# Optimization experiments

Hardware: AMD Instinct MI355X
Metric: run time of the kernel (lower is better)

## Reference

```python
import jax, jax.numpy as jnp
import numpy as np

N_BLADES = 32  # Cl(4,1) has 2^5 = 32 basis blades


def _gp_sign_bitwise(a, b):
    """Sign of e_a * e_b in Cl(4,1) via bitwise swap counting (numpy, static)."""
    a = np.asarray(a, dtype=np.int64)
    b = np.asarray(b, dtype=np.int64)
    a, b = np.broadcast_arrays(a, b)
    swaps = np.zeros(a.shape, dtype=np.int64)
    for i in range(5):
        b_has_i = (b >> i) & 1
        mask_gt = (~((1 << (i + 1)) - 1)) & 31
        val = a & mask_gt
        pc = (val & 1) + ((val >> 1) & 1) + ((val >> 2) & 1) + ((val >> 3) & 1) + ((val >> 4) & 1)
        swaps += b_has_i * pc
    comm_sign = np.where(swaps % 2 == 0, 1.0, -1.0)
    metric_sign = np.where(((a & 16) & (b & 16)) > 0, -1.0, 1.0)
    return (comm_sign * metric_sign).astype(np.float32)


_M = np.arange(N_BLADES)
PERM = (_M[:, None] ^ _M[None, :]).astype(np.int32)        # PERM[k, m] = m ^ k
SIGNS = _gp_sign_bitwise(_M[None, :], PERM)                 # sign(m, m^k), [32, 32]
PERM_J = jnp.asarray(PERM)
SIGNS_J = jnp.asarray(SIGNS)


def setup_inputs() -> dict:
    key = jax.random.key(0)
    kx, kw = jax.random.split(key)
    B, In, Out = 1024, 256, 256
    x = jax.random.normal(kx, (B, In, N_BLADES), dtype=jnp.float32)
    std = 0.5 / (In * N_BLADES) ** 0.5
    weight = jax.random.normal(kw, (Out, In, N_BLADES), dtype=jnp.float32) * std
    return {"x": x, "weight": weight}


def reference(x, weight):
    # x: [B, In, 32], weight: [Out, In, 32]
    # out[b, o, k] = sum_{i, m} x[b, i, m^k] * sign(m, m^k) * w[o, i, m]
    x_g = x[..., PERM_J] * SIGNS_J                 # [B, In, 32(k), 32(m)]
    out = jnp.einsum('bikm,oim->bok', x_g, weight)  # [B, Out, 32]
    return out
```

## Files before the change

kernel.cpp:

```cpp
#include <hip/hip_runtime.h>

typedef __attribute__((ext_vector_type(8))) short bf16x8;
typedef __attribute__((ext_vector_type(4))) float f32x4;
typedef __attribute__((ext_vector_type(8))) unsigned short ushort8;

#define N_BLADES 32
#define B_DIM 1024
#define IN_DIM 256
#define OUT_DIM 256
#define K_DIM (IN_DIM * N_BLADES)
#define N_DIM (OUT_DIM * N_BLADES)


__device__ __forceinline__ unsigned short f2bf(float f) {
    unsigned int u = __float_as_uint(f);
    u = (u + 0x7fff + ((u >> 16) & 1)) >> 16;
    return (unsigned short)u;
}

__device__ __forceinline__ float gp_sign(int a, int b) {
    int swaps = 0;
#pragma unroll
    for (int i = 0; i < 5; ++i) {
        int mask = (~((1 << (i + 1)) - 1)) & 31;
        swaps += ((b >> i) & 1) * __popc(a & mask);
    }
    float s = (swaps & 1) ? -1.0f : 1.0f;
    if (a & b & 16) s = -s;
    return s;
}

__device__ __forceinline__ void gload_lds16(const void* g, void* l) {
    __builtin_amdgcn_global_load_lds(
        (const __attribute__((address_space(1))) unsigned int*)g,
        (__attribute__((address_space(3))) unsigned int*)l, 16, 0, 0);
}

#define FENCE() asm volatile("" ::: "memory")
#define BAR()    { FENCE(); __builtin_amdgcn_s_barrier(); FENCE(); }
#define SCHED0() __builtin_amdgcn_sched_barrier(0)
#define LGKM(n)  { asm volatile("s_waitcnt lgkmcnt(" #n ")" ::: "memory"); SCHED0(); }
#define VMC(n)   { asm volatile("s_waitcnt vmcnt(" #n ")" ::: "memory"); SCHED0(); }
#define PRIO1()  __builtin_amdgcn_s_setprio(1)
#define PRIO0()  __builtin_amdgcn_s_setprio(0)

__global__ __launch_bounds__(256) void cast_kernel(const float4* __restrict__ x,
                                                   unsigned short* __restrict__ xb) {
    int t = blockIdx.x * 256 + threadIdx.x;
    float4 a = x[t * 2];
    float4 b = x[t * 2 + 1];
    ushort8 pk;
    pk[0] = f2bf(a.x); pk[1] = f2bf(a.y); pk[2] = f2bf(a.z); pk[3] = f2bf(a.w);
    pk[4] = f2bf(b.x); pk[5] = f2bf(b.y); pk[6] = f2bf(b.z); pk[7] = f2bf(b.w);
    *(ushort8*)(xb + (size_t)t * 8) = pk;
}

__device__ __forceinline__ bf16x8 shuffle_sign(bf16x8 v, int jx,
                                               unsigned int m0, unsigned int m1,
                                               unsigned int m2, unsigned int m3) {
    union { bf16x8 v8; unsigned int w[4]; } a, b;
    a.v8 = v;
    int s = jx >> 1;
    unsigned int t0 = (s & 1) ? a.w[1] : a.w[0];
    unsigned int t1 = (s & 1) ? a.w[0] : a.w[1];
    unsigned int t2 = (s & 1) ? a.w[3] : a.w[2];
    unsigned int t3 = (s & 1) ? a.w[2] : a.w[3];
    unsigned int u0 = (s & 2) ? t2 : t0;
    unsigned int u1 = (s & 2) ? t3 : t1;
    unsigned int u2 = (s & 2) ? t0 : t2;
    unsigned int u3 = (s & 2) ? t1 : t3;
    if (jx & 1) {
        u0 = (u0 >> 16) | (u0 << 16);
        u1 = (u1 >> 16) | (u1 << 16);
        u2 = (u2 >> 16) | (u2 << 16);
        u3 = (u3 >> 16) | (u3 << 16);
    }
    b.w[0] = u0 ^ m0; b.w[1] = u1 ^ m1; b.w[2] = u2 ^ m2; b.w[3] = u3 ^ m3;
    return b.v8;
}


#define ABUF 16384
#define TBUF 49152
#define ROWB 16384

__global__ __launch_bounds__(512, 1) void gemm_ko_kernel(const unsigned short* __restrict__ xb,
                                                         const unsigned short* __restrict__ wb,
                                                         float* __restrict__ Cws) {
    __shared__ char lds[3 * TBUF];

    const int tid  = threadIdx.x;
    const int lane = tid & 63;
    const int wid  = tid >> 6;
    const int wr   = wid >> 2;
    const int wc   = wid & 3;
    const int l15  = lane & 15;
    const int l4   = lane >> 4;
    const int swzf = (l15 & 7) << 4;

    const int  kblk = blockIdx.x;
    const long row0 = (long)blockIdx.y * 128;
    const int  jx   = kblk & 7;
    const int  khi  = kblk & 24;

    const int rowA = tid >> 2;
    const int h0   = (2 * tid) & 7;
    const int q0   = h0 & 3, q1 = (h0 + 1) & 3;
    const int aoff0 = ((h0 >> 2) * 64) + (((q0 * 8) ^ khi) * 2);
    const int aoff1 = (((h0 + 1) >> 2) * 64) + (((q1 * 8) ^ khi) * 2);
    const int adst0 = rowA * 128 + ((h0 * 16) ^ ((rowA & 7) << 4));
    const int adst1 = rowA * 128 + (((h0 + 1) * 16) ^ ((rowA & 7) << 4));
    const char* aSrcK = (const char*)xb + (row0 + rowA) * ROWB;

    unsigned int mA00, mA01, mA02, mA03, mA10, mA11, mA12, mA13;
    {
        unsigned int mk[2][4];
#pragma unroll
        for (int u = 0; u < 2; ++u) {
            int q = u ? q1 : q0;
#pragma unroll
            for (int w = 0; w < 4; ++w) {
                unsigned int mword = 0;
#pragma unroll
                for (int e2 = 0; e2 < 2; ++e2) {
                    int m = 8 * q + 2 * w + e2;
                    if (gp_sign(m, m ^ kblk) < 0.0f) mword |= 0x8000u << (16 * e2);
                }
                mk[u][w] = mword;
            }
        }
        mA00 = mk[0][0]; mA01 = mk[0][1]; mA02 = mk[0][2]; mA03 = mk[0][3];
        mA10 = mk[1][0]; mA11 = mk[1][1]; mA12 = mk[1][2]; mA13 = mk[1][3];
    }

    const int  rrB   = tid >> 3;
    const int  tid16 = tid * 16;
    const int  scbB  = ((tid & 7) * 16) ^ ((rrB & 7) << 4);
    const char* bSrc = (const char*)wb + (long)rrB * ROWB + scbB;

    char* buf0 = lds;
    char* buf1 = lds + TBUF;
    char* buf2 = lds + 2 * TBUF;

#define B_STAGE(nbuf, kpb) { \
    _Pragma("unroll") for (int n = 0; n < 4; ++n) \
        gload_lds16(bSrc + (long)n * (64L * ROWB) + (kpb), (char*)(nbuf) + ABUF + n * 8192 + tid16); }
#define A_LOAD(kpb) { \
    rA0 = *(const bf16x8*)(aSrcK + (kpb) + aoff0); \
    rA1 = *(const bf16x8*)(aSrcK + (kpb) + aoff1); }
#define A_SHUF_WRITE(nbuf) { \
    bf16x8 s0 = shuffle_sign(rA0, jx, mA00, mA01, mA02, mA03); \
    bf16x8 s1 = shuffle_sign(rA1, jx, mA10, mA11, mA12, mA13); \
    *(bf16x8*)((char*)(nbuf) + adst0) = s0; \
    *(bf16x8*)((char*)(nbuf) + adst1) = s1; }
#define READ_AB(pbuf, kk, AS, BS) { \
    _Pragma("unroll") for (int mi = 0; mi < 4; ++mi) { \
        int r = wr * 64 + mi * 16 + l15; \
        AS[mi] = *(const bf16x8*)((const char*)(pbuf) + r * 128 + (((kk) * 64 + l4 * 16) ^ swzf)); } \
    _Pragma("unroll") for (int ni = 0; ni < 4; ++ni) { \
        int r = wc * 64 + ni * 16 + l15; \
        BS[ni] = *(const bf16x8*)((const char*)(pbuf) + ABUF + r * 128 + (((kk) * 64 + l4 * 16) ^ swzf)); } }
#define MFMA16(AS, BS) \
    _Pragma("unroll") for (int mi = 0; mi < 4; ++mi) \
    _Pragma("unroll") for (int ni = 0; ni < 4; ++ni) \
        acc[mi][ni] = __builtin_amdgcn_mfma_f32_16x16x32_bf16(AS[mi], BS[ni], acc[mi][ni], 0, 0, 0);

    f32x4 acc[4][4];
#pragma unroll
    for (int mi = 0; mi < 4; ++mi)
#pragma unroll
        for (int ni = 0; ni < 4; ++ni) acc[mi][ni] = (f32x4)0.0f;

    bf16x8 rA0, rA1;
    bf16x8 aF0[4], bF0[4], aF1[4], bF1[4];

    A_LOAD(0);
    VMC(0);
    A_SHUF_WRITE(buf0);
    SCHED0();
    B_STAGE(buf0, 0);
    SCHED0();
    A_LOAD(128);
    SCHED0();
    B_STAGE(buf1, 128);
    SCHED0();
    VMC(6);
    LGKM(0);
    BAR();

    char* pc = buf0; char* pn = buf1; char* ps = buf2;
    int kp = 256;
    for (int t = 0; t < 128; ++t) {
        READ_AB(pc, 0, aF0, bF0);
        SCHED0();
        READ_AB(pc, 1, aF1, bF1);
        VMC(4);
        A_SHUF_WRITE(pn);
        SCHED0();
        A_LOAD(kp);
        SCHED0();
        B_STAGE(ps, kp);
        SCHED0();
        LGKM(10); PRIO1(); MFMA16(aF0, bF0); PRIO0();
        LGKM(2);  PRIO1(); MFMA16(aF1, bF1); PRIO0();
        VMC(6);
        LGKM(0);
        BAR();

        char* tmp = pc; pc = pn; pn = ps; ps = tmp;
        kp += 128;
        if (kp == 16384) kp = 0;
    }

    const int cr = l4 * 4;
#pragma unroll
    for (int mi = 0; mi < 4; ++mi)
#pragma unroll
        for (int ni = 0; ni < 4; ++ni)
#pragma unroll
            for (int jj = 0; jj < 4; ++jj) {
                long r = row0 + wr * 64 + mi * 16 + cr + jj;
                int  c = kblk * 256 + wc * 64 + ni * 16 + l15;
                Cws[r * N_DIM + c] = acc[mi][ni][jj];
            }

#undef B_STAGE
#undef A_LOAD
#undef A_SHUF_WRITE
#undef READ_AB
#undef MFMA16
}

__global__ __launch_bounds__(256) void transpose_kernel(const float* __restrict__ Cws,
                                                        float* __restrict__ out) {
    __shared__ float t[32 * 260];
    const int tid = threadIdx.x;
    const long b  = blockIdx.x;
    const float4* src = (const float4*)(Cws + b * N_DIM);
    float4*       dst = (float4*)(out + b * N_DIM);
#pragma unroll
    for (int r = 0; r < 8; ++r) {
        int f = tid + r * 256;
        float4 v = src[f];
        int k  = f >> 6;
        int c4 = (f & 63) * 4;
        *(float4*)&t[k * 260 + c4] = v;
    }
    __syncthreads();
#pragma unroll
    for (int r = 0; r < 8; ++r) {
        int g  = tid + r * 256;
        int o  = g >> 3;
        int k0 = (g & 7) * 4;
        float4 v;
        v.x = t[(k0 + 0) * 260 + o];
        v.y = t[(k0 + 1) * 260 + o];
        v.z = t[(k0 + 2) * 260 + o];
        v.w = t[(k0 + 3) * 260 + o];
        dst[g] = v;
    }
}

__global__ __launch_bounds__(256) void fallback_gp_kernel(const float* __restrict__ x,
                                                          const float* __restrict__ w,
                                                          float* __restrict__ out) {
    __shared__ float xs[IN_DIM * 32];
    __shared__ float tab[1024];
    int tid = threadIdx.x;
    for (int idx = tid; idx < 1024; idx += 256) {
        int m = idx >> 5, k = idx & 31;
        tab[idx] = gp_sign(m, m ^ k);
    }
    int b = blockIdx.x;
    const float4* xrow = (const float4*)(x + (long)b * K_DIM);
    float4* xs4 = (float4*)xs;
    for (int idx = tid; idx < 2048; idx += 256) xs4[idx] = xrow[idx];
    __syncthreads();

    int wid = tid >> 6, lane = tid & 63;
    int o = blockIdx.y * 8 + wid;
    int k = lane & 31, half = lane >> 5;
    float acc = 0.f;
    const float* wrow = w + (long)o * K_DIM + half * 4096;
    for (int i = 0; i < 128; ++i) {
        int ib = (half * 128 + i) * 32;
#pragma unroll
        for (int m = 0; m < 32; ++m) {
            acc += xs[ib + (m ^ k)] * tab[m * 32 + k] * wrow[i * 32 + m];
        }
    }
    acc += __shfl_down(acc, 32);
    if (half == 0) out[((long)b * OUT_DIM + o) * 32 + k] = acc;
}

extern "C" void kernel_launch(void* const* d_in, const int* in_sizes, int n_in,
                              void* d_out, int out_size, void* d_ws, size_t ws_size,
                              hipStream_t stream) {
    const float* x = (const float*)d_in[0];
    const float* w = (const float*)d_in[1];
    float* out = (float*)d_out;

    const size_t xb_bytes  = (size_t)B_DIM * K_DIM * 2;
    const size_t wb_bytes  = (size_t)OUT_DIM * IN_DIM * 32 * 2;
    const size_t cw_bytes  = (size_t)B_DIM * N_DIM * 4;
    const size_t need = xb_bytes + wb_bytes + cw_bytes;

    if (ws_size >= need) {
        unsigned short* xbp = (unsigned short*)d_ws;
        unsigned short* wbp = (unsigned short*)((char*)d_ws + xb_bytes);
        float*          cws = (float*)((char*)d_ws + xb_bytes + wb_bytes);

        cast_kernel<<<dim3(4096), dim3(256), 0, stream>>>((const float4*)x, xbp);
        cast_kernel<<<dim3(1024), dim3(256), 0, stream>>>((const float4*)w, wbp);
        gemm_ko_kernel<<<dim3(32, 8), dim3(512), 0, stream>>>(xbp, wbp, cws);
        transpose_kernel<<<dim3(B_DIM), dim3(256), 0, stream>>>(cws, out);
    } else {
        fallback_gp_kernel<<<dim3(B_DIM, OUT_DIM / 8), dim3(256), 0, stream>>>(x, w, out);
    }
}
```

Before: 155.1 us.

## Split GEMM into 128x128 tiles with 256-thread blocks and double buffering

The GEMM kernel moves from 512-thread blocks computing 128x256 tiles with triple-buffered LDS to 256-thread blocks computing 128x128 tiles with double-buffered LDS. The grid gains a column dimension, so there are 512 blocks instead of 256, and launch bounds now allow two blocks per CU. The loop is restructured so the next B stage is issued before the MFMAs and the A shuffle-write is interleaved between the two MFMA halves. The aim is better occupancy and more blocks to fill the CUs. In exchange, A tiles are loaded and sign-shuffled twice as often and the pipeline is shallower.

```diff
diff --git a/kernel.cpp b/kernel.cpp
--- a/kernel.cpp
+++ b/kernel.cpp
@@ -80,90 +80,90 @@
 }
 
 
-#define ABUF 16384
-#define TBUF 49152
 #define ROWB 16384
-
-__global__ __launch_bounds__(512, 1) void gemm_ko_kernel(const unsigned short* __restrict__ xb,
-                                                         const unsigned short* __restrict__ wb,
-                                                         float* __restrict__ Cws) {
-    __shared__ char lds[3 * TBUF];
+#define BOFF 16384
+#define BUFB 32768
+
+__global__ __launch_bounds__(256, 2) void gemm_ko2_kernel(const unsigned short* __restrict__ xb,
+                                                          const unsigned short* __restrict__ wb,
+                                                          float* __restrict__ Cws) {
+    __shared__ char lds[2 * BUFB];
 
     const int tid  = threadIdx.x;
     const int lane = tid & 63;
     const int wid  = tid >> 6;
-    const int wr   = wid >> 2;
-    const int wc   = wid & 3;
+    const int wr   = wid >> 1;
+    const int wc   = wid & 1;
     const int l15  = lane & 15;
     const int l4   = lane >> 4;
     const int swzf = (l15 & 7) << 4;
 
     const int  kblk = blockIdx.x;
-    const long row0 = (long)blockIdx.y * 128;
+    const long col0 = (long)blockIdx.y * 128;
+    const long row0 = (long)blockIdx.z * 128;
     const int  jx   = kblk & 7;
     const int  khi  = kblk & 24;
 
-    const int rowA = tid >> 2;
-    const int h0   = (2 * tid) & 7;
-    const int q0   = h0 & 3, q1 = (h0 + 1) & 3;
-    const int aoff0 = ((h0 >> 2) * 64) + (((q0 * 8) ^ khi) * 2);
-    const int aoff1 = (((h0 + 1) >> 2) * 64) + (((q1 * 8) ^ khi) * 2);
-    const int adst0 = rowA * 128 + ((h0 * 16) ^ ((rowA & 7) << 4));
-    const int adst1 = rowA * 128 + (((h0 + 1) * 16) ^ ((rowA & 7) << 4));
-    const char* aSrcK = (const char*)xb + (row0 + rowA) * ROWB;
-
-    unsigned int mA00, mA01, mA02, mA03, mA10, mA11, mA12, mA13;
-    {
-        unsigned int mk[2][4];
-#pragma unroll
-        for (int u = 0; u < 2; ++u) {
-            int q = u ? q1 : q0;
-#pragma unroll
-            for (int w = 0; w < 4; ++w) {
-                unsigned int mword = 0;
-#pragma unroll
-                for (int e2 = 0; e2 < 2; ++e2) {
-                    int m = 8 * q + 2 * w + e2;
-                    if (gp_sign(m, m ^ kblk) < 0.0f) mword |= 0x8000u << (16 * e2);
-                }
-                mk[u][w] = mword;
+    const int rA8   = tid >> 1;
+    const int hbase = (tid & 1) * 4;
+    const int isub  = (tid & 1);
+    const char* aSrcX = (const char*)xb + (row0 + rA8) * ROWB;
+    const int aoff0 = isub * 64 + (((0 * 8) ^ khi) * 2);
+    const int aoff1 = isub * 64 + (((1 * 8) ^ khi) * 2);
+    const int aoff2 = isub * 64 + (((2 * 8) ^ khi) * 2);
+    const int aoff3 = isub * 64 + (((3 * 8) ^ khi) * 2);
+    const int aswz  = (rA8 & 7) << 4;
+    const int adst0 = rA8 * 128 + (((hbase + 0) * 16) ^ aswz);
+    const int adst1 = rA8 * 128 + (((hbase + 1) * 16) ^ aswz);
+    const int adst2 = rA8 * 128 + (((hbase + 2) * 16) ^ aswz);
+    const int adst3 = rA8 * 128 + (((hbase + 3) * 16) ^ aswz);
+
+    unsigned int mk[4][4];
+#pragma unroll
+    for (int n = 0; n < 4; ++n)
+#pragma unroll
+        for (int w_ = 0; w_ < 4; ++w_) {
+            unsigned int mw = 0;
+#pragma unroll
+            for (int e2 = 0; e2 < 2; ++e2) {
+                int m = 8 * n + 2 * w_ + e2;
+                if (gp_sign(m, m ^ kblk) < 0.0f) mw |= 0x8000u << (16 * e2);
             }
+            mk[n][w_] = mw;
         }
-        mA00 = mk[0][0]; mA01 = mk[0][1]; mA02 = mk[0][2]; mA03 = mk[0][3];
-        mA10 = mk[1][0]; mA11 = mk[1][1]; mA12 = mk[1][2]; mA13 = mk[1][3];
-    }
-
-    const int  rrB   = tid >> 3;
+
     const int  tid16 = tid * 16;
-    const int  scbB  = ((tid & 7) * 16) ^ ((rrB & 7) << 4);
-    const char* bSrc = (const char*)wb + (long)rrB * ROWB + scbB;
-
-    char* buf0 = lds;
-    char* buf1 = lds + TBUF;
-    char* buf2 = lds + 2 * TBUF;
+    const char* bSrcW = (const char*)wb + (col0 + (tid >> 3)) * ROWB
+                        + (((tid & 7) * 16) ^ (((tid >> 3) & 7) << 4));
 
 #define B_STAGE(nbuf, kpb) { \
     _Pragma("unroll") for (int n = 0; n < 4; ++n) \
-        gload_lds16(bSrc + (long)n * (64L * ROWB) + (kpb), (char*)(nbuf) + ABUF + n * 8192 + tid16); }
+        gload_lds16(bSrcW + (long)n * (32L * ROWB) + (kpb), (char*)(nbuf) + BOFF + n * 4096 + tid16); }
 #define A_LOAD(kpb) { \
-    rA0 = *(const bf16x8*)(aSrcK + (kpb) + aoff0); \
-    rA1 = *(const bf16x8*)(aSrcK + (kpb) + aoff1); }
+    rA0_ = *(const bf16x8*)(aSrcX + (kpb) + aoff0); \
+    rA1_ = *(const bf16x8*)(aSrcX + (kpb) + aoff1); \
+    rA2_ = *(const bf16x8*)(aSrcX + (kpb) + aoff2); \
+    rA3_ = *(const bf16x8*)(aSrcX + (kpb) + aoff3); }
 #define A_SHUF_WRITE(nbuf) { \
-    bf16x8 s0 = shuffle_sign(rA0, jx, mA00, mA01, mA02, mA03); \
-    bf16x8 s1 = shuffle_sign(rA1, jx, mA10, mA11, mA12, mA13); \
-    *(bf16x8*)((char*)(nbuf) + adst0) = s0; \
-    *(bf16x8*)((char*)(nbuf) + adst1) = s1; }
-#define READ_AB(pbuf, kk, AS, BS) { \
+    bf16x8 s0_ = shuffle_sign(rA0_, jx, mk[0][0], mk[0][1], mk[0][2], mk[0][3]); \
+    bf16x8 s1_ = shuffle_sign(rA1_, jx, mk[1][0], mk[1][1], mk[1][2], mk[1][3]); \
+    bf16x8 s2_ = shuffle_sign(rA2_, jx, mk[2][0], mk[2][1], mk[2][2], mk[2][3]); \
+    bf16x8 s3_ = shuffle_sign(rA3_, jx, mk[3][0], mk[3][1], mk[3][2], mk[3][3]); \
+    *(bf16x8*)((char*)(nbuf) + adst0) = s0_; \
+    *(bf16x8*)((char*)(nbuf) + adst1) = s1_; \
+    *(bf16x8*)((char*)(nbuf) + adst2) = s2_; \
+    *(bf16x8*)((char*)(nbuf) + adst3) = s3_; }
+#define READ8(pbuf, kk) { \
     _Pragma("unroll") for (int mi = 0; mi < 4; ++mi) { \
         int r = wr * 64 + mi * 16 + l15; \
-        AS[mi] = *(const bf16x8*)((const char*)(pbuf) + r * 128 + (((kk) * 64 + l4 * 16) ^ swzf)); } \
+        aF[kk][mi] = *(const bf16x8*)((const char*)(pbuf) + r * 128 + (((kk) * 64 + l4 * 16) ^ swzf)); } \
     _Pragma("unroll") for (int ni = 0; ni < 4; ++ni) { \
         int r = wc * 64 + ni * 16 + l15; \
-        BS[ni] = *(const bf16x8*)((const char*)(pbuf) + ABUF + r * 128 + (((kk) * 64 + l4 * 16) ^ swzf)); } }
-#define MFMA16(AS, BS) \
+        bF[kk][ni] = *(const bf16x8*)((const char*)(pbuf) + BOFF + r * 128 + (((kk) * 64 + l4 * 16) ^ swzf)); } }
+#define MFMA16(kk) \
     _Pragma("unroll") for (int mi = 0; mi < 4; ++mi) \
     _Pragma("unroll") for (int ni = 0; ni < 4; ++ni) \
-        acc[mi][ni] = __builtin_amdgcn_mfma_f32_16x16x32_bf16(AS[mi], BS[ni], acc[mi][ni], 0, 0, 0);
+        acc[mi][ni] = __builtin_amdgcn_mfma_f32_16x16x32_bf16(aF[kk][mi], bF[kk][ni], acc[mi][ni], 0, 0, 0);
 
     f32x4 acc[4][4];
 #pragma unroll
@@ -171,8 +171,11 @@
 #pragma unroll
         for (int ni = 0; ni < 4; ++ni) acc[mi][ni] = (f32x4)0.0f;
 
-    bf16x8 rA0, rA1;
-    bf16x8 aF0[4], bF0[4], aF1[4], bF1[4];
+    bf16x8 rA0_, rA1_, rA2_, rA3_;
+    bf16x8 aF[2][4], bF[2][4];
+
+    char* buf0 = lds;
+    char* buf1 = lds + BUFB;
 
     A_LOAD(0);
     VMC(0);
@@ -182,34 +185,33 @@
     SCHED0();
     A_LOAD(128);
     SCHED0();
-    B_STAGE(buf1, 128);
-    SCHED0();
-    VMC(6);
     LGKM(0);
+    VMC(4);
     BAR();
 
-    char* pc = buf0; char* pn = buf1; char* ps = buf2;
-    int kp = 256;
     for (int t = 0; t < 128; ++t) {
-        READ_AB(pc, 0, aF0, bF0);
+        char* pc = (t & 1) ? buf1 : buf0;
+        char* pn = (t & 1) ? buf0 : buf1;
+        const int kpn = ((t + 1) & 127) * 128;
+        const int kp2 = ((t + 2) & 127) * 128;
+
+        READ8(pc, 0);
         SCHED0();
-        READ_AB(pc, 1, aF1, bF1);
+        B_STAGE(pn, kpn);
+        SCHED0();
+        READ8(pc, 1);
+        LGKM(8);
+        PRIO1(); MFMA16(0); PRIO0();
         VMC(4);
         A_SHUF_WRITE(pn);
         SCHED0();
-        A_LOAD(kp);
+        A_LOAD(kp2);
         SCHED0();
-        B_STAGE(ps, kp);
-        SCHED0();
-        LGKM(10); PRIO1(); MFMA16(aF0, bF0); PRIO0();
-        LGKM(2);  PRIO1(); MFMA16(aF1, bF1); PRIO0();
-        VMC(6);
+        LGKM(4);
+        PRIO1(); MFMA16(1); PRIO0();
         LGKM(0);
+        VMC(4);
         BAR();
-
-        char* tmp = pc; pc = pn; pn = ps; ps = tmp;
-        kp += 128;
-        if (kp == 16384) kp = 0;
     }
 
     const int cr = l4 * 4;
@@ -220,14 +222,14 @@
 #pragma unroll
             for (int jj = 0; jj < 4; ++jj) {
                 long r = row0 + wr * 64 + mi * 16 + cr + jj;
-                int  c = kblk * 256 + wc * 64 + ni * 16 + l15;
+                long c = (long)kblk * 256 + col0 + wc * 64 + ni * 16 + l15;
                 Cws[r * N_DIM + c] = acc[mi][ni][jj];
             }
 
 #undef B_STAGE
 #undef A_LOAD
 #undef A_SHUF_WRITE
-#undef READ_AB
+#undef READ8
 #undef MFMA16
 }
 
@@ -312,7 +314,7 @@
 
         cast_kernel<<<dim3(4096), dim3(256), 0, stream>>>((const float4*)x, xbp);
         cast_kernel<<<dim3(1024), dim3(256), 0, stream>>>((const float4*)w, wbp);
-        gemm_ko_kernel<<<dim3(32, 8), dim3(512), 0, stream>>>(xbp, wbp, cws);
+        gemm_ko2_kernel<<<dim3(32, 2, 8), dim3(256), 0, stream>>>(xbp, wbp, cws);
         transpose_kernel<<<dim3(B_DIM), dim3(256), 0, stream>>>(cws, out);
     } else {
         fallback_gp_kernel<<<dim3(B_DIM, OUT_DIM / 8), dim3(256), 0, stream>>>(x, w, out);
```

Result: slower. 179.2 us (+15.5%).

## Switch GEMM to 32x32x16 MFMA with deeper B pipeline and split A buffers

Applied to the files above, without the earlier changes.

Replaces the 16x16x32 bf16 MFMA tiling with 32x32x16 MFMAs (2x2 tiles of f32x16 accumulators per wave). This halves the number of LDS fragment reads per MFMA flop. The LDS layout becomes two A buffers plus four B buffers, so B is prefetched three tiles ahead, and the loop is unrolled by four with even/odd A register sets. It also drops the s_setprio hints and the sched barriers inside the waitcnt macros, and changes the wait counts. The risks are higher register pressure, more LDS use, and wait-count tuning that may leave the pipeline imbalanced.

```diff
diff --git a/kernel.cpp b/kernel.cpp
--- a/kernel.cpp
+++ b/kernel.cpp
@@ -1,7 +1,7 @@
 #include <hip/hip_runtime.h>
 
 typedef __attribute__((ext_vector_type(8))) short bf16x8;
-typedef __attribute__((ext_vector_type(4))) float f32x4;
+typedef __attribute__((ext_vector_type(16))) float f32x16;
 typedef __attribute__((ext_vector_type(8))) unsigned short ushort8;
 
 #define N_BLADES 32
@@ -39,10 +39,8 @@
 #define FENCE() asm volatile("" ::: "memory")
 #define BAR()    { FENCE(); __builtin_amdgcn_s_barrier(); FENCE(); }
 #define SCHED0() __builtin_amdgcn_sched_barrier(0)
-#define LGKM(n)  { asm volatile("s_waitcnt lgkmcnt(" #n ")" ::: "memory"); SCHED0(); }
-#define VMC(n)   { asm volatile("s_waitcnt vmcnt(" #n ")" ::: "memory"); SCHED0(); }
-#define PRIO1()  __builtin_amdgcn_s_setprio(1)
-#define PRIO0()  __builtin_amdgcn_s_setprio(0)
+#define LGKM(n)  { asm volatile("s_waitcnt lgkmcnt(" #n ")" ::: "memory"); }
+#define VMC(n)   { asm volatile("s_waitcnt vmcnt(" #n ")" ::: "memory"); }
 
 __global__ __launch_bounds__(256) void cast_kernel(const float4* __restrict__ x,
                                                    unsigned short* __restrict__ xb) {
@@ -80,23 +78,21 @@
 }
 
 
-#define ABUF 16384
-#define TBUF 49152
 #define ROWB 16384
 
-__global__ __launch_bounds__(512, 1) void gemm_ko_kernel(const unsigned short* __restrict__ xb,
-                                                         const unsigned short* __restrict__ wb,
-                                                         float* __restrict__ Cws) {
-    __shared__ char lds[3 * TBUF];
+__global__ __launch_bounds__(512, 1) void gemm_ko32_kernel(const unsigned short* __restrict__ xb,
+                                                           const unsigned short* __restrict__ wb,
+                                                           float* __restrict__ Cws) {
+    __shared__ char lds[163840];
 
     const int tid  = threadIdx.x;
     const int lane = tid & 63;
     const int wid  = tid >> 6;
     const int wr   = wid >> 2;
     const int wc   = wid & 3;
-    const int l15  = lane & 15;
-    const int l4   = lane >> 4;
-    const int swzf = (l15 & 7) << 4;
+    const int l31  = lane & 31;
+    const int l5   = lane >> 5;
+    const int swzf = (l31 & 7) << 4;
 
     const int  kblk = blockIdx.x;
     const long row0 = (long)blockIdx.y * 128;
@@ -105,11 +101,12 @@
 
     const int rowA = tid >> 2;
     const int h0   = (2 * tid) & 7;
-    const int q0   = h0 & 3, q1 = (h0 + 1) & 3;
+    const int q0 = h0 & 3, q1 = (h0 + 1) & 3;
     const int aoff0 = ((h0 >> 2) * 64) + (((q0 * 8) ^ khi) * 2);
     const int aoff1 = (((h0 + 1) >> 2) * 64) + (((q1 * 8) ^ khi) * 2);
-    const int adst0 = rowA * 128 + ((h0 * 16) ^ ((rowA & 7) << 4));
-    const int adst1 = rowA * 128 + (((h0 + 1) * 16) ^ ((rowA & 7) << 4));
+    const int aswz  = (rowA & 7) << 4;
+    const int adst0 = rowA * 128 + ((h0 * 16) ^ aswz);
+    const int adst1 = rowA * 128 + (((h0 + 1) * 16) ^ aswz);
     const char* aSrcK = (const char*)xb + (row0 + rowA) * ROWB;
 
     unsigned int mA00, mA01, mA02, mA03, mA10, mA11, mA12, mA13;
@@ -119,116 +116,158 @@
         for (int u = 0; u < 2; ++u) {
             int q = u ? q1 : q0;
 #pragma unroll
-            for (int w = 0; w < 4; ++w) {
-                unsigned int mword = 0;
+            for (int w_ = 0; w_ < 4; ++w_) {
+                unsigned int mw = 0;
 #pragma unroll
                 for (int e2 = 0; e2 < 2; ++e2) {
-                    int m = 8 * q + 2 * w + e2;
-                    if (gp_sign(m, m ^ kblk) < 0.0f) mword |= 0x8000u << (16 * e2);
+                    int m = 8 * q + 2 * w_ + e2;
+                    if (gp_sign(m, m ^ kblk) < 0.0f) mw |= 0x8000u << (16 * e2);
                 }
-                mk[u][w] = mword;
+                mk[u][w_] = mw;
             }
         }
         mA00 = mk[0][0]; mA01 = mk[0][1]; mA02 = mk[0][2]; mA03 = mk[0][3];
         mA10 = mk[1][0]; mA11 = mk[1][1]; mA12 = mk[1][2]; mA13 = mk[1][3];
     }
 
-    const int  rrB   = tid >> 3;
     const int  tid16 = tid * 16;
-    const int  scbB  = ((tid & 7) * 16) ^ ((rrB & 7) << 4);
-    const char* bSrc = (const char*)wb + (long)rrB * ROWB + scbB;
-
-    char* buf0 = lds;
-    char* buf1 = lds + TBUF;
-    char* buf2 = lds + 2 * TBUF;
-
-#define B_STAGE(nbuf, kpb) { \
+    const char* bSrc = (const char*)wb + (long)(tid >> 3) * ROWB
+                       + (((tid & 7) * 16) ^ (((tid >> 3) & 7) << 4));
+
+    const int aRdB = (wr * 64 + l31) * 128;
+    const int bRdB = (wc * 64 + l31) * 128;
+    const int col0_ = ((0 * 32) + l5 * 16) ^ swzf;
+    const int col1_ = ((1 * 32) + l5 * 16) ^ swzf;
+    const int col2_ = ((2 * 32) + l5 * 16) ^ swzf;
+    const int col3_ = ((3 * 32) + l5 * 16) ^ swzf;
+
+#define B_STAGE(br, kpb) { \
     _Pragma("unroll") for (int n = 0; n < 4; ++n) \
-        gload_lds16(bSrc + (long)n * (64L * ROWB) + (kpb), (char*)(nbuf) + ABUF + n * 8192 + tid16); }
-#define A_LOAD(kpb) { \
-    rA0 = *(const bf16x8*)(aSrcK + (kpb) + aoff0); \
-    rA1 = *(const bf16x8*)(aSrcK + (kpb) + aoff1); }
-#define A_SHUF_WRITE(nbuf) { \
-    bf16x8 s0 = shuffle_sign(rA0, jx, mA00, mA01, mA02, mA03); \
-    bf16x8 s1 = shuffle_sign(rA1, jx, mA10, mA11, mA12, mA13); \
-    *(bf16x8*)((char*)(nbuf) + adst0) = s0; \
-    *(bf16x8*)((char*)(nbuf) + adst1) = s1; }
-#define READ_AB(pbuf, kk, AS, BS) { \
-    _Pragma("unroll") for (int mi = 0; mi < 4; ++mi) { \
-        int r = wr * 64 + mi * 16 + l15; \
-        AS[mi] = *(const bf16x8*)((const char*)(pbuf) + r * 128 + (((kk) * 64 + l4 * 16) ^ swzf)); } \
-    _Pragma("unroll") for (int ni = 0; ni < 4; ++ni) { \
-        int r = wc * 64 + ni * 16 + l15; \
-        BS[ni] = *(const bf16x8*)((const char*)(pbuf) + ABUF + r * 128 + (((kk) * 64 + l4 * 16) ^ swzf)); } }
-#define MFMA16(AS, BS) \
-    _Pragma("unroll") for (int mi = 0; mi < 4; ++mi) \
-    _Pragma("unroll") for (int ni = 0; ni < 4; ++ni) \
-        acc[mi][ni] = __builtin_amdgcn_mfma_f32_16x16x32_bf16(AS[mi], BS[ni], acc[mi][ni], 0, 0, 0);
-
-    f32x4 acc[4][4];
-#pragma unroll
-    for (int mi = 0; mi < 4; ++mi)
-#pragma unroll
-        for (int ni = 0; ni < 4; ++ni) acc[mi][ni] = (f32x4)0.0f;
-
-    bf16x8 rA0, rA1;
-    bf16x8 aF0[4], bF0[4], aF1[4], bF1[4];
-
-    A_LOAD(0);
-    VMC(0);
-    A_SHUF_WRITE(buf0);
-    SCHED0();
-    B_STAGE(buf0, 0);
-    SCHED0();
-    A_LOAD(128);
-    SCHED0();
-    B_STAGE(buf1, 128);
+        gload_lds16(bSrc + (long)n * (64L * ROWB) + (kpb), \
+                    lds + 32768 + (br) * 32768 + n * 8192 + tid16); }
+#define A_LOAD_E(kpb) { \
+    rAe0 = *(const bf16x8*)(aSrcK + (kpb) + aoff0); \
+    rAe1 = *(const bf16x8*)(aSrcK + (kpb) + aoff1); }
+#define A_LOAD_O(kpb) { \
+    rAo0 = *(const bf16x8*)(aSrcK + (kpb) + aoff0); \
+    rAo1 = *(const bf16x8*)(aSrcK + (kpb) + aoff1); }
+#define A_WRITE_E(ab) { \
+    bf16x8 s0_ = shuffle_sign(rAe0, jx, mA00, mA01, mA02, mA03); \
+    bf16x8 s1_ = shuffle_sign(rAe1, jx, mA10, mA11, mA12, mA13); \
+    *(bf16x8*)(lds + (ab) * 16384 + adst0) = s0_; \
+    *(bf16x8*)(lds + (ab) * 16384 + adst1) = s1_; }
+#define A_WRITE_O(ab) { \
+    bf16x8 s0_ = shuffle_sign(rAo0, jx, mA00, mA01, mA02, mA03); \
+    bf16x8 s1_ = shuffle_sign(rAo1, jx, mA10, mA11, mA12, mA13); \
+    *(bf16x8*)(lds + (ab) * 16384 + adst0) = s0_; \
+    *(bf16x8*)(lds + (ab) * 16384 + adst1) = s1_; }
+
+#define READ_G0(ab, br) { \
+    aG0[0][0] = *(const bf16x8*)(lds + (ab)*16384 + aRdB + 0*4096 + col0_); \
+    aG0[0][1] = *(const bf16x8*)(lds + (ab)*16384 + aRdB + 0*4096 + col1_); \
+    aG0[1][0] = *(const bf16x8*)(lds + (ab)*16384 + aRdB + 1*4096 + col0_); \
+    aG0[1][1] = *(const bf16x8*)(lds + (ab)*16384 + aRdB + 1*4096 + col1_); \
+    bG0[0][0] = *(const bf16x8*)(lds + 32768 + (br)*32768 + bRdB + 0*4096 + col0_); \
+    bG0[0][1] = *(const bf16x8*)(lds + 32768 + (br)*32768 + bRdB + 0*4096 + col1_); \
+    bG0[1][0] = *(const bf16x8*)(lds + 32768 + (br)*32768 + bRdB + 1*4096 + col0_); \
+    bG0[1][1] = *(const bf16x8*)(lds + 32768 + (br)*32768 + bRdB + 1*4096 + col1_); }
+#define READ_G1(ab, br) { \
+    aG1[0][0] = *(const bf16x8*)(lds + (ab)*16384 + aRdB + 0*4096 + col2_); \
+    aG1[0][1] = *(const bf16x8*)(lds + (ab)*16384 + aRdB + 0*4096 + col3_); \
+    aG1[1][0] = *(const bf16x8*)(lds + (ab)*16384 + aRdB + 1*4096 + col2_); \
+    aG1[1][1] = *(const bf16x8*)(lds + (ab)*16384 + aRdB + 1*4096 + col3_); \
+    bG1[0][0] = *(const bf16x8*)(lds + 32768 + (br)*32768 + bRdB + 0*4096 + col2_); \
+    bG1[0][1] = *(const bf16x8*)(lds + 32768 + (br)*32768 + bRdB + 0*4096 + col3_); \
+    bG1[1][0] = *(const bf16x8*)(lds + 32768 + (br)*32768 + bRdB + 1*4096 + col2_); \
+    bG1[1][1] = *(const bf16x8*)(lds + 32768 + (br)*32768 + bRdB + 1*4096 + col3_); }
+#define MFG0() \
+    _Pragma("unroll") for (int s = 0; s < 2; ++s) \
+    _Pragma("unroll") for (int mt = 0; mt < 2; ++mt) \
+    _Pragma("unroll") for (int nt = 0; nt < 2; ++nt) \
+        acc[mt][nt] = __builtin_amdgcn_mfma_f32_32x32x16_bf16(aG0[mt][s], bG0[nt][s], acc[mt][nt], 0, 0, 0);
+#define MFG1() \
+    _Pragma("unroll") for (int s = 0; s < 2; ++s) \
+    _Pragma("unroll") for (int mt = 0; mt < 2; ++mt) \
+    _Pragma("unroll") for (int nt = 0; nt < 2; ++nt) \
+        acc[mt][nt] = __builtin_amdgcn_mfma_f32_32x32x16_bf16(aG1[mt][s], bG1[nt][s], acc[mt][nt], 0, 0, 0);
+
+    f32x16 acc[2][2];
+#pragma unroll
+    for (int mt = 0; mt < 2; ++mt)
+#pragma unroll
+        for (int nt = 0; nt < 2; ++nt) acc[mt][nt] = (f32x16)0.0f;
+
+    bf16x8 rAe0, rAe1, rAo0, rAo1;
+    bf16x8 aG0[2][2], bG0[2][2], aG1[2][2], bG1[2][2];
+
+    A_LOAD_E(0);
+    SCHED0();
+    B_STAGE(0, 0);
+    B_STAGE(1, 128);
+    SCHED0();
+    VMC(8);
+    A_WRITE_E(0);
+    SCHED0();
+    A_LOAD_O(128);
+    SCHED0();
+    B_STAGE(2, 256);
     SCHED0();
     VMC(6);
     LGKM(0);
     BAR();
 
-    char* pc = buf0; char* pn = buf1; char* ps = buf2;
-    int kp = 256;
-    for (int t = 0; t < 128; ++t) {
-        READ_AB(pc, 0, aF0, bF0);
-        SCHED0();
-        READ_AB(pc, 1, aF1, bF1);
-        VMC(4);
-        A_SHUF_WRITE(pn);
-        SCHED0();
-        A_LOAD(kp);
-        SCHED0();
-        B_STAGE(ps, kp);
-        SCHED0();
-        LGKM(10); PRIO1(); MFMA16(aF0, bF0); PRIO0();
-        LGKM(2);  PRIO1(); MFMA16(aF1, bF1); PRIO0();
-        VMC(6);
-        LGKM(0);
-        BAR();
-
-        char* tmp = pc; pc = pn; pn = ps; ps = tmp;
-        kp += 128;
-        if (kp == 16384) kp = 0;
-    }
-
-    const int cr = l4 * 4;
-#pragma unroll
-    for (int mi = 0; mi < 4; ++mi)
-#pragma unroll
-        for (int ni = 0; ni < 4; ++ni)
-#pragma unroll
-            for (int jj = 0; jj < 4; ++jj) {
-                long r = row0 + wr * 64 + mi * 16 + cr + jj;
-                int  c = kblk * 256 + wc * 64 + ni * 16 + l15;
-                Cws[r * N_DIM + c] = acc[mi][ni][jj];
+#define TILE32(AB, ABN, BR, BRS, ALOAD, AWRITE, Texp) { \
+    const int T_ = (Texp); \
+    const int kAr = ((T_ + 2) & 127) << 7; \
+    const int kBg = ((T_ + 3) & 127) << 7; \
+    READ_G0(AB, BR); \
+    SCHED0(); \
+    READ_G1(AB, BR); \
+    SCHED0(); \
+    ALOAD(kAr);             \
+    SCHED0(); \
+    B_STAGE(BRS, kBg);      \
+    SCHED0(); \
+    LGKM(8); MFG0(); \
+    VMC(10);                \
+    AWRITE(ABN); \
+    SCHED0(); \
+    LGKM(2); MFG1(); \
+    LGKM(0); \
+    VMC(6);                 \
+    BAR(); }
+
+    for (int t = 0; t < 32; ++t) {
+        const int T4 = t * 4;
+        TILE32(0, 1, 0, 3, A_LOAD_E, A_WRITE_O, T4);
+        TILE32(1, 0, 1, 0, A_LOAD_O, A_WRITE_E, T4 + 1);
+        TILE32(0, 1, 2, 1, A_LOAD_E, A_WRITE_O, T4 + 2);
+        TILE32(1, 0, 3, 2, A_LOAD_O, A_WRITE_E, T4 + 3);
+    }
+
+#pragma unroll
+    for (int mt = 0; mt < 2; ++mt)
+#pragma unroll
+        for (int nt = 0; nt < 2; ++nt) {
+            long c = (long)kblk * 256 + wc * 64 + nt * 32 + l31;
+#pragma unroll
+            for (int r = 0; r < 16; ++r) {
+                int  rl = (r & 3) + 8 * (r >> 2) + 4 * l5;
+                long rb = row0 + wr * 64 + mt * 32 + rl;
+                Cws[rb * N_DIM + c] = acc[mt][nt][r];
             }
+        }
 
 #undef B_STAGE
-#undef A_LOAD
-#undef A_SHUF_WRITE
-#undef READ_AB
-#undef MFMA16
+#undef A_LOAD_E
+#undef A_LOAD_O
+#undef A_WRITE_E
+#undef A_WRITE_O
+#undef READ_G0
+#undef READ_G1
+#undef MFG0
+#undef MFG1
+#undef TILE32
 }
 
 __global__ __launch_bounds__(256) void transpose_kernel(const float* __restrict__ Cws,
@@ -312,7 +351,7 @@
 
         cast_kernel<<<dim3(4096), dim3(256), 0, stream>>>((const float4*)x, xbp);
         cast_kernel<<<dim3(1024), dim3(256), 0, stream>>>((const float4*)w, wbp);
-        gemm_ko_kernel<<<dim3(32, 8), dim3(512), 0, stream>>>(xbp, wbp, cws);
+        gemm_ko32_kernel<<<dim3(32, 8), dim3(512), 0, stream>>>(xbp, wbp, cws);
         transpose_kernel<<<dim3(B_DIM), dim3(256), 0, stream>>>(cws, out);
     } else {
         fallback_gp_kernel<<<dim3(B_DIM, OUT_DIM / 8), dim3(256), 0, stream>>>(x, w, out);
```

Result: slower. 176.9 us (+14.0%).
